# Performance work log

Hardware: AMD Instinct MI355X
Metric: run time of the kernel (lower is better)

The kernel has to match this reference:

```python
import jax, jax.numpy as jnp
import numpy as np

N_SRC = 50000
N_DST = 50000
N_EDGES = 600000
IN_FEAT = 128
OUT_FEAT = 128


def setup_inputs() -> dict:
    key = jax.random.key(0)
    k1, k2, k3, k4, k5, k6 = jax.random.split(key, 6)
    h_s = jax.random.normal(k1, (N_SRC, IN_FEAT), dtype=jnp.float32)
    h_d = jax.random.normal(k2, (N_DST, IN_FEAT), dtype=jnp.float32)
    src = jax.random.randint(k3, (N_EDGES,), 0, N_SRC, dtype=jnp.int32)
    dst = jax.random.randint(k4, (N_EDGES,), 0, N_DST, dtype=jnp.int32)
    # nn.Linear(in_feat*2, out_feat): W [out, 2*in], b [out]
    W = jax.random.normal(k5, (OUT_FEAT, 2 * IN_FEAT), dtype=jnp.float32) * 0.05
    b = jax.random.normal(k6, (OUT_FEAT,), dtype=jnp.float32) * 0.05
    return {"h_s": h_s, "h_d": h_d, "src": src, "dst": dst, "W": W, "b": b}


def reference(h_s, h_d, src, dst, W, b):
    # copy_u + mean: gather source features along edges, segment-mean by dst
    msgs = h_s[src]  # [E, in_feat]
    neigh_sum = jax.ops.segment_sum(msgs, dst, num_segments=N_DST)  # [n_dst, in_feat]
    deg = jax.ops.segment_sum(jnp.ones((src.shape[0],), dtype=h_s.dtype), dst,
                              num_segments=N_DST)
    h_neigh = neigh_sum / jnp.maximum(deg, 1.0)[:, None]  # zero-degree -> 0
    # concat + linear (dropout is identity in eval mode)
    feat = jnp.concatenate([h_d, h_neigh], axis=1)  # [n_dst, 2*in_feat]
    out = feat @ W.T + b  # [n_dst, out_feat]
    return out
```

## Files before the change

### kernel.cpp

```cpp
#include <hip/hip_runtime.h>
#include <hip/hip_bf16.h>

#define N_SRC 50000
#define N_DST 50000
#define N_EDGES 600000
#define IN_FEAT 128
#define OUT_FEAT 128
#define CAP 64

typedef __attribute__((ext_vector_type(8))) short short8;
typedef __attribute__((ext_vector_type(4))) float float4v;
typedef __attribute__((ext_vector_type(4))) float f32x4;
typedef __attribute__((ext_vector_type(4))) unsigned short ushort4v;

#define FILL_BLOCKS ((N_EDGES + 255) / 256)
#define HS4 (N_SRC * IN_FEAT / 4)
#define CVT_BLOCKS (HS4 / 256)
#define W_BLOCKS 16
#define K1_GRID (FILL_BLOCKS + 2 * CVT_BLOCKS + W_BLOCKS)

__global__ __launch_bounds__(256) void fill_cvt_kernel(
    const float* __restrict__ h_s, const float* __restrict__ h_d,
    const float* __restrict__ W,
    const int* __restrict__ src, const int* __restrict__ dst,
    int* __restrict__ deg, ushort* __restrict__ permu,
    ushort* __restrict__ hsb, ushort* __restrict__ hdb,
    ushort* __restrict__ wfrag)
{
    int bid = blockIdx.x;
    int tid = threadIdx.x;

    if (bid < FILL_BLOCKS) {
        int e = bid * 256 + tid;
        if (e < N_EDGES) {
            int s = __builtin_nontemporal_load(src + e);
            int d = __builtin_nontemporal_load(dst + e);
            int p = atomicAdd(&deg[d], 1);
            if (p < CAP) permu[(size_t)d * CAP + p] = (ushort)s;
        }
        return;
    }
    bid -= FILL_BLOCKS;

    if (bid < 2 * CVT_BLOCKS) {
        bool first = (bid < CVT_BLOCKS);
        const float* in = first ? h_s : h_d;
        ushort* outp    = first ? hsb : hdb;
        int idx = (first ? bid : bid - CVT_BLOCKS) * 256 + tid;
        f32x4 v = __builtin_nontemporal_load((const f32x4*)in + idx);
        __hip_bfloat16 o[4];
        o[0] = __float2bfloat16(v.x);
        o[1] = __float2bfloat16(v.y);
        o[2] = __float2bfloat16(v.z);
        o[3] = __float2bfloat16(v.w);
        __builtin_nontemporal_store(*(ushort4v*)o, (ushort4v*)(outp + (size_t)idx * 4));
        return;
    }
    bid -= 2 * CVT_BLOCKS;

    int c = bid * 256 + tid;
    int f  = c >> 6;
    int l  = c & 63;
    int ks = f >> 3;
    int nt = f & 7;
    int row = nt * 16 + (l & 15);
    int col = ks * 32 + (l >> 4) * 8;
    const float* wp = W + (size_t)row * 256 + col;
    f32x4 w0 = __builtin_nontemporal_load((const f32x4*)wp);
    f32x4 w1 = __builtin_nontemporal_load((const f32x4*)wp + 1);
    __hip_bfloat16 o[8];
    o[0] = __float2bfloat16(w0.x); o[1] = __float2bfloat16(w0.y);
    o[2] = __float2bfloat16(w0.z); o[3] = __float2bfloat16(w0.w);
    o[4] = __float2bfloat16(w1.x); o[5] = __float2bfloat16(w1.y);
    o[6] = __float2bfloat16(w1.z); o[7] = __float2bfloat16(w1.w);
    __builtin_nontemporal_store(*(short8*)o, (short8*)(wfrag + (size_t)c * 8));
}

__global__ __launch_bounds__(256) void gather_kernel(
    const ushort* __restrict__ hsb, const int* __restrict__ deg,
    const ushort* __restrict__ permu, ushort* __restrict__ neighb)
{
    int wave = threadIdx.x >> 6;
    int lane = threadIdx.x & 63;
    int row  = blockIdx.x * 4 + wave;
    if (row >= N_DST) return;

    int dg  = deg[row];
    int dgr = (dg < CAP) ? dg : CAP;
    const ushort* prow = permu + (size_t)row * CAP;

    float ax = 0.f, ay = 0.f;
    {
        ushort4 p0 = *(const ushort4*)(prow);
        ushort4 p1 = *(const ushort4*)(prow + 4);
        ushort4 p2 = *(const ushort4*)(prow + 8);
        ushort4 p3 = *(const ushort4*)(prow + 12);
        int t[16] = {p0.x, p0.y, p0.z, p0.w, p1.x, p1.y, p1.z, p1.w,
                     p2.x, p2.y, p2.z, p2.w, p3.x, p3.y, p3.z, p3.w};
        ushort2 u[16];
#pragma unroll
        for (int q = 0; q < 16; ++q) {
            int s = (q < dgr) ? t[q] : 0;
            u[q] = ((const ushort2*)(hsb + (size_t)s * IN_FEAT))[lane];
        }
#pragma unroll
        for (int q = 0; q < 16; ++q) {
            float m = (q < dgr) ? 1.f : 0.f;
            ax += m * __uint_as_float((unsigned)u[q].x << 16);
            ay += m * __uint_as_float((unsigned)u[q].y << 16);
        }
    }
    for (int j = 16; j < dgr; j += 8) {
        ushort4 pa = *(const ushort4*)(prow + j);
        ushort4 pb = *(const ushort4*)(prow + j + 4);
        int t[8] = {pa.x, pa.y, pa.z, pa.w, pb.x, pb.y, pb.z, pb.w};
        ushort2 u[8];
#pragma unroll
        for (int q = 0; q < 8; ++q) {
            int s = (j + q < dgr) ? t[q] : 0;
            u[q] = ((const ushort2*)(hsb + (size_t)s * IN_FEAT))[lane];
        }
#pragma unroll
        for (int q = 0; q < 8; ++q) {
            float m = (j + q < dgr) ? 1.f : 0.f;
            ax += m * __uint_as_float((unsigned)u[q].x << 16);
            ay += m * __uint_as_float((unsigned)u[q].y << 16);
        }
    }
    float inv = (dg > 0) ? (1.0f / (float)dg) : 0.0f;
    __hip_bfloat16 ox = __float2bfloat16(ax * inv);
    __hip_bfloat16 oy = __float2bfloat16(ay * inv);
    unsigned pk = (unsigned)*(ushort*)&ox | ((unsigned)*(ushort*)&oy << 16);
    __builtin_nontemporal_store(pk, (unsigned*)(neighb + (size_t)row * IN_FEAT) + lane);
}

__global__ __launch_bounds__(256) void gemm_mfma_kernel(
    const ushort* __restrict__ hdb, const ushort* __restrict__ neighb,
    const ushort* __restrict__ wfrag, const float* __restrict__ b,
    float* __restrict__ out)
{
    int tid  = threadIdx.x;
    int wave = tid >> 6;
    int lane = tid & 63;
    int lm   = lane & 15;
    int lq   = lane >> 4;

    int row0 = blockIdx.x * 64 + wave * 16;
    int ar   = row0 + lm;  ar = (ar < N_DST) ? ar : (N_DST - 1);
    const ushort* ah = hdb    + (size_t)ar * IN_FEAT + lq * 8;
    const ushort* an = neighb + (size_t)ar * IN_FEAT + lq * 8;

    float4v acc[8];
#pragma unroll
    for (int nt = 0; nt < 8; ++nt) acc[nt] = (float4v){0.f, 0.f, 0.f, 0.f};

#pragma unroll
    for (int ks = 0; ks < 8; ++ks) {
        int koff = (ks & 3) * 32;
        short8 af = (ks < 4)
            ? __builtin_nontemporal_load((const short8*)(ah + koff))
            : __builtin_nontemporal_load((const short8*)(an + koff));
#pragma unroll
        for (int nt = 0; nt < 8; ++nt) {
            short8 bf = *(const short8*)(wfrag + ((size_t)(ks * 8 + nt) * 64 + lane) * 8);
            acc[nt] = __builtin_amdgcn_mfma_f32_16x16x32_bf16(af, bf, acc[nt], 0, 0, 0);
        }
    }

    int orow0 = row0 + lq * 4;
#pragma unroll
    for (int nt = 0; nt < 8; ++nt) {
        int col = nt * 16 + lm;
        float bias = b[col];
#pragma unroll
        for (int r = 0; r < 4; ++r) {
            int o = orow0 + r;
            if (o < N_DST)
                __builtin_nontemporal_store(acc[nt][r] + bias,
                                            out + (size_t)o * OUT_FEAT + col);
        }
    }
}

extern "C" void kernel_launch(void* const* d_in, const int* in_sizes, int n_in,
                              void* d_out, int out_size, void* d_ws, size_t ws_size,
                              hipStream_t stream) {
    const float* h_s = (const float*)d_in[0];
    const float* h_d = (const float*)d_in[1];
    const int*   src = (const int*)d_in[2];
    const int*   dst = (const int*)d_in[3];
    const float* W   = (const float*)d_in[4];
    const float* b   = (const float*)d_in[5];
    float* out = (float*)d_out;

    char* ws = (char*)d_ws;
    int*    deg    = (int*)ws;
    ushort* permu  = (ushort*)(ws + 200000);
    ushort* hsb    = (ushort*)(ws + 6600000);
    ushort* hdb    = (ushort*)(ws + 19400000);
    ushort* neighb = (ushort*)(ws + 32200000);
    ushort* wfrag  = (ushort*)(ws + 45000000);

    hipMemsetAsync(deg, 0, N_DST * sizeof(int), stream);

    fill_cvt_kernel<<<K1_GRID, 256, 0, stream>>>(
        h_s, h_d, W, src, dst, deg, permu, hsb, hdb, wfrag);
    gather_kernel<<<(N_DST + 3) / 4, 256, 0, stream>>>(
        hsb, deg, permu, neighb);
    gemm_mfma_kernel<<<(N_DST + 63) / 64, 256, 0, stream>>>(
        hdb, neighb, wfrag, b, out);
}
```

Before: 178.8 us.

## Fuse neighbor gather and MFMA GEMM into one kernel via shared memory

Merges the gather/mean kernel and the GEMM kernel into a single kernel. Each block gathers the neighbor means for 16 destination rows into XOR-swizzled LDS, then its four waves each compute two 16-column output tiles with MFMA. This drops the bf16 neighb round trip through global memory and one kernel launch. The cost is that each wave now serially gathers 4 rows and there is a block barrier before the GEMM, which may reduce latency hiding.

New measurement: 176.7 us. Within noise of the previous version (-1.2%).

```diff
diff --git a/kernel.cpp b/kernel.cpp
--- a/kernel.cpp
+++ b/kernel.cpp
@@ -76,32 +76,42 @@
     __builtin_nontemporal_store(*(short8*)o, (short8*)(wfrag + (size_t)c * 8));
 }
 
-__global__ __launch_bounds__(256) void gather_kernel(
+__global__ __launch_bounds__(256) void gather_gemm_kernel(
     const ushort* __restrict__ hsb, const int* __restrict__ deg,
-    const ushort* __restrict__ permu, ushort* __restrict__ neighb)
+    const ushort* __restrict__ permu, const ushort* __restrict__ hdb,
+    const ushort* __restrict__ wfrag, const float* __restrict__ b,
+    float* __restrict__ out)
 {
-    int wave = threadIdx.x >> 6;
-    int lane = threadIdx.x & 63;
-    int row  = blockIdx.x * 4 + wave;
-    if (row >= N_DST) return;
-
-    int dg  = deg[row];
-    int dgr = (dg < CAP) ? dg : CAP;
-    const ushort* prow = permu + (size_t)row * CAP;
-
-    float ax = 0.f, ay = 0.f;
-    {
+    __shared__ ushort sM[16 * 128];
+
+    int tid  = threadIdx.x;
+    int wave = tid >> 6;
+    int lane = tid & 63;
+    int lm   = lane & 15;
+    int lq   = lane >> 4;
+    int row0 = blockIdx.x * 16;
+
+    for (int r = 0; r < 4; ++r) {
+        int lr  = wave * 4 + r;
+        int row = row0 + lr;
+        int dg  = deg[row];
+        int dgr = (dg < CAP) ? dg : CAP;
+        const ushort* prow = permu + (size_t)row * CAP;
+        const ushort2* hp  = (const ushort2*)hsb;
+
         ushort4 p0 = *(const ushort4*)(prow);
         ushort4 p1 = *(const ushort4*)(prow + 4);
         ushort4 p2 = *(const ushort4*)(prow + 8);
         ushort4 p3 = *(const ushort4*)(prow + 12);
         int t[16] = {p0.x, p0.y, p0.z, p0.w, p1.x, p1.y, p1.z, p1.w,
                      p2.x, p2.y, p2.z, p2.w, p3.x, p3.y, p3.z, p3.w};
+
+        float ax = 0.f, ay = 0.f;
         ushort2 u[16];
 #pragma unroll
         for (int q = 0; q < 16; ++q) {
             int s = (q < dgr) ? t[q] : 0;
-            u[q] = ((const ushort2*)(hsb + (size_t)s * IN_FEAT))[lane];
+            u[q] = hp[(size_t)s * 64 + lane];
         }
 #pragma unroll
         for (int q = 0; q < 16; ++q) {
@@ -109,75 +119,67 @@
             ax += m * __uint_as_float((unsigned)u[q].x << 16);
             ay += m * __uint_as_float((unsigned)u[q].y << 16);
         }
-    }
-    for (int j = 16; j < dgr; j += 8) {
-        ushort4 pa = *(const ushort4*)(prow + j);
-        ushort4 pb = *(const ushort4*)(prow + j + 4);
-        int t[8] = {pa.x, pa.y, pa.z, pa.w, pb.x, pb.y, pb.z, pb.w};
-        ushort2 u[8];
-#pragma unroll
-        for (int q = 0; q < 8; ++q) {
-            int s = (j + q < dgr) ? t[q] : 0;
-            u[q] = ((const ushort2*)(hsb + (size_t)s * IN_FEAT))[lane];
-        }
-#pragma unroll
-        for (int q = 0; q < 8; ++q) {
-            float m = (j + q < dgr) ? 1.f : 0.f;
-            ax += m * __uint_as_float((unsigned)u[q].x << 16);
-            ay += m * __uint_as_float((unsigned)u[q].y << 16);
-        }
-    }
-    float inv = (dg > 0) ? (1.0f / (float)dg) : 0.0f;
-    __hip_bfloat16 ox = __float2bfloat16(ax * inv);
-    __hip_bfloat16 oy = __float2bfloat16(ay * inv);
-    unsigned pk = (unsigned)*(ushort*)&ox | ((unsigned)*(ushort*)&oy << 16);
-    __builtin_nontemporal_store(pk, (unsigned*)(neighb + (size_t)row * IN_FEAT) + lane);
-}
-
-__global__ __launch_bounds__(256) void gemm_mfma_kernel(
-    const ushort* __restrict__ hdb, const ushort* __restrict__ neighb,
-    const ushort* __restrict__ wfrag, const float* __restrict__ b,
-    float* __restrict__ out)
-{
-    int tid  = threadIdx.x;
-    int wave = tid >> 6;
-    int lane = tid & 63;
-    int lm   = lane & 15;
-    int lq   = lane >> 4;
-
-    int row0 = blockIdx.x * 64 + wave * 16;
-    int ar   = row0 + lm;  ar = (ar < N_DST) ? ar : (N_DST - 1);
-    const ushort* ah = hdb    + (size_t)ar * IN_FEAT + lq * 8;
-    const ushort* an = neighb + (size_t)ar * IN_FEAT + lq * 8;
-
-    float4v acc[8];
-#pragma unroll
-    for (int nt = 0; nt < 8; ++nt) acc[nt] = (float4v){0.f, 0.f, 0.f, 0.f};
+        for (int j = 16; j < dgr; j += 8) {
+            ushort4 pa = *(const ushort4*)(prow + j);
+            ushort4 pb = *(const ushort4*)(prow + j + 4);
+            int tt[8] = {pa.x, pa.y, pa.z, pa.w, pb.x, pb.y, pb.z, pb.w};
+            ushort2 v[8];
+#pragma unroll
+            for (int q = 0; q < 8; ++q) {
+                int s = (j + q < dgr) ? tt[q] : 0;
+                v[q] = hp[(size_t)s * 64 + lane];
+            }
+#pragma unroll
+            for (int q = 0; q < 8; ++q) {
+                float m = (j + q < dgr) ? 1.f : 0.f;
+                ax += m * __uint_as_float((unsigned)v[q].x << 16);
+                ay += m * __uint_as_float((unsigned)v[q].y << 16);
+            }
+        }
+
+        float inv = (dg > 0) ? (1.0f / (float)dg) : 0.0f;
+        __hip_bfloat16 ox = __float2bfloat16(ax * inv);
+        __hip_bfloat16 oy = __float2bfloat16(ay * inv);
+        unsigned pk = (unsigned)*(ushort*)&ox | ((unsigned)*(ushort*)&oy << 16);
+        unsigned byte = ((unsigned)(lr * 256 + lane * 4)) ^ (((unsigned)lr & 7u) << 4);
+        *(unsigned*)((char*)sM + byte) = pk;
+    }
+    __syncthreads();
+
+    const ushort* ah = hdb + (size_t)(row0 + lm) * IN_FEAT + lq * 8;
+
+    float4v acc[2];
+    acc[0] = (float4v){0.f, 0.f, 0.f, 0.f};
+    acc[1] = (float4v){0.f, 0.f, 0.f, 0.f};
 
 #pragma unroll
     for (int ks = 0; ks < 8; ++ks) {
-        int koff = (ks & 3) * 32;
-        short8 af = (ks < 4)
-            ? __builtin_nontemporal_load((const short8*)(ah + koff))
-            : __builtin_nontemporal_load((const short8*)(an + koff));
-#pragma unroll
-        for (int nt = 0; nt < 8; ++nt) {
+        short8 af;
+        if (ks < 4) {
+            af = __builtin_nontemporal_load((const short8*)(ah + ks * 32));
+        } else {
+            unsigned byte = ((unsigned)(lm * 256 + (((ks - 4) * 32 + lq * 8) * 2)))
+                            ^ (((unsigned)lm & 7u) << 4);
+            af = *(const short8*)((char*)sM + byte);
+        }
+#pragma unroll
+        for (int j = 0; j < 2; ++j) {
+            int nt = wave * 2 + j;
             short8 bf = *(const short8*)(wfrag + ((size_t)(ks * 8 + nt) * 64 + lane) * 8);
-            acc[nt] = __builtin_amdgcn_mfma_f32_16x16x32_bf16(af, bf, acc[nt], 0, 0, 0);
-        }
-    }
-
-    int orow0 = row0 + lq * 4;
-#pragma unroll
-    for (int nt = 0; nt < 8; ++nt) {
+            acc[j] = __builtin_amdgcn_mfma_f32_16x16x32_bf16(af, bf, acc[j], 0, 0, 0);
+        }
+    }
+
+#pragma unroll
+    for (int j = 0; j < 2; ++j) {
+        int nt  = wave * 2 + j;
         int col = nt * 16 + lm;
         float bias = b[col];
 #pragma unroll
         for (int r = 0; r < 4; ++r) {
-            int o = orow0 + r;
-            if (o < N_DST)
-                __builtin_nontemporal_store(acc[nt][r] + bias,
-                                            out + (size_t)o * OUT_FEAT + col);
+            int o = row0 + lq * 4 + r;
+            __builtin_nontemporal_store(acc[j][r] + bias,
+                                        out + (size_t)o * OUT_FEAT + col);
         }
     }
 }
@@ -198,15 +200,12 @@
     ushort* permu  = (ushort*)(ws + 200000);
     ushort* hsb    = (ushort*)(ws + 6600000);
     ushort* hdb    = (ushort*)(ws + 19400000);
-    ushort* neighb = (ushort*)(ws + 32200000);
-    ushort* wfrag  = (ushort*)(ws + 45000000);
+    ushort* wfrag  = (ushort*)(ws + 32200000);
 
     hipMemsetAsync(deg, 0, N_DST * sizeof(int), stream);
 
     fill_cvt_kernel<<<K1_GRID, 256, 0, stream>>>(
         h_s, h_d, W, src, dst, deg, permu, hsb, hdb, wfrag);
-    gather_kernel<<<(N_DST + 3) / 4, 256, 0, stream>>>(
-        hsb, deg, permu, neighb);
-    gemm_mfma_kernel<<<(N_DST + 63) / 64, 256, 0, stream>>>(
-        hdb, neighb, wfrag, b, out);
+    gather_gemm_kernel<<<N_DST / 16, 256, 0, stream>>>(
+        hsb, deg, permu, hdb, wfrag, b, out);
 }
```
